# Kernel tuning notes

Hardware: AMD Instinct MI355X
Metric: run time of the kernel (lower is better)

Reference implementation:

```python
import jax, jax.numpy as jnp
import numpy as np

N = 8  # fixed node count per sample (hardcoded in the torch module)


def setup_inputs() -> dict:
    key = jax.random.key(0)
    ks = jax.random.split(key, 13)
    B = 131072

    def w(k, shape, fan_in):
        # torch nn.Linear default init: U(-1/sqrt(fan_in), 1/sqrt(fan_in))
        return jax.random.uniform(k, shape, jnp.float32, -1.0, 1.0) / np.sqrt(fan_in).astype(np.float32)

    return {
        "x": jax.random.normal(ks[0], (B, N), jnp.float32),
        "enc_w1": w(ks[1], (3, 64), 3),   "enc_b1": w(ks[2], (64,), 3),
        "enc_w2": w(ks[3], (64, 2), 64),  "enc_b2": w(ks[4], (2,), 64),
        "gcn1_w": w(ks[5], (2, 32), 2),   "gcn1_b": w(ks[6], (32,), 2),
        "gcn2_w": w(ks[7], (32, 32), 32), "gcn2_b": w(ks[8], (32,), 32),
        "dec_w1": w(ks[9], (32, 64), 32), "dec_b1": w(ks[10], (64,), 32),
        "dec_w2": w(ks[11], (64, 3), 64), "dec_b2": w(ks[12], (3,), 64),
    }


def _gabriel_norm_adj(p):
    """Batched Gabriel graph -> GCN-normalized (A + I) with unit edge weights.

    p: (B, N, 2) latent 2D points.
    Edge (i,j) exists iff no other point k lies strictly inside the circle
    with diameter (p_i, p_j)  (dist(p_k, mid)^2 < r^2, matching torch's '<').
    Gabriel graphs contain the nearest-neighbor graph, so for N>=2 edges always
    exist and the torch fallback branch is unreachable.
    Returns D^{-1/2} (A + I) D^{-1/2} of shape (B, N, N) (GCNConv default:
    add_self_loops=True with weight 1, symmetric normalization).
    """
    mid = (p[:, :, None, :] + p[:, None, :, :]) * 0.5                 # (B,N,N,2)
    r2 = jnp.sum((p[:, :, None, :] - mid) ** 2, axis=-1)              # (B,N,N)
    # d2[b,i,j,k] = ||p[b,k] - mid[b,i,j]||^2  -> (B,N,N,N), the big intermediate
    d2 = jnp.sum((p[:, None, None, :, :] - mid[:, :, :, None, :]) ** 2, axis=-1)
    a = jnp.arange(N)
    k_not_ij = (a[None, None, :] != a[:, None, None]) & (a[None, None, :] != a[None, :, None])  # (N,N,N) [i,j,k]
    blocked = jnp.any((d2 < r2[..., None]) & k_not_ij, axis=-1)       # (B,N,N)
    off_diag = a[:, None] != a[None, :]
    adj = ((~blocked) & off_diag).astype(p.dtype)                     # symmetric Gabriel adjacency
    a_hat = adj + jnp.eye(N, dtype=p.dtype)                           # self-loops, weight 1
    dinv = jax.lax.rsqrt(jnp.sum(a_hat, axis=-1))                     # (B,N)
    return dinv[:, :, None] * a_hat * dinv[:, None, :]


def reference(x, enc_w1, enc_b1, enc_w2, enc_b2,
              gcn1_w, gcn1_b, gcn2_w, gcn2_b,
              dec_w1, dec_b1, dec_w2, dec_b2):
    B = x.shape[0]
    idx = jnp.arange(N, dtype=x.dtype)
    # preprocess: (B, N, 3) rows [0, value, index]
    xp = jnp.stack([jnp.zeros_like(x), x, jnp.broadcast_to(idx, x.shape)], axis=-1)
    latent = jax.nn.relu(xp @ enc_w1 + enc_b1) @ enc_w2 + enc_b2      # (B,N,2)
    # torch builds the graph from detach().cpu().numpy() -> no grad through structure
    norm = jax.lax.stop_gradient(_gabriel_norm_adj(latent))           # (B,N,N)
    h1 = jax.nn.relu(jnp.einsum('bij,bjf->bif', norm, latent @ gcn1_w) + gcn1_b)  # (B,N,32)
    h2 = jnp.einsum('bij,bjf->bif', norm, h1 @ gcn2_w) + gcn2_b                    # (B,N,32)
    pooled = jnp.mean(h2, axis=1)                                     # (B,32)
    node = jnp.broadcast_to(pooled[:, None, :], (B, N, pooled.shape[-1]))
    dec = jax.nn.relu(node @ dec_w1 + dec_b1) @ dec_w2 + dec_b2       # (B,N,3)
    reconstructed = dec[:, :, 1]                                      # (B,N)
    return reconstructed, latent
```

## Files before the change

kernel.cpp:

```cpp
#include <hip/hip_runtime.h>


typedef float v2 __attribute__((ext_vector_type(2)));
static __device__ __forceinline__ v2 sp(float s) { return (v2){s, s}; }
static __device__ __forceinline__ v2 fma2(v2 a, v2 b, v2 c) {
    return __builtin_elementwise_fma(a, b, c);
}
static __device__ __forceinline__ v2 ldv2(const float* p) {
    return *reinterpret_cast<const v2*>(p);
}

__global__ __launch_bounds__(256) void gae_aux(
    const float* __restrict__ gcn2_w, const float* __restrict__ gcn2_b,
    const float* __restrict__ dec_w1, const float* __restrict__ dec_b1,
    const float* __restrict__ dec_w2, const float* __restrict__ enc_w1,
    const float* __restrict__ enc_b1, float* __restrict__ ws)
{
    const int tid = blockIdx.x * 256 + threadIdx.x;
    const int f = tid >> 6, h = tid & 63;
    float acc = 0.0f;
    #pragma unroll 8
    for (int g = 0; g < 32; ++g)
        acc = fmaf(gcn2_w[f * 32 + g], dec_w1[g * 64 + h], acc);
    ws[f * 64 + h] = acc;
    if (tid < 64) {
        float c = dec_b1[h];
        #pragma unroll 8
        for (int g = 0; g < 32; ++g)
            c = fmaf(gcn2_b[g], dec_w1[g * 64 + h], c);
        ws[2048 + h] = c;
        ws[2112 + h] = dec_w2[h * 3 + 1];
    }
    if (tid < 512) {
        const int hh = tid >> 3, ii = tid & 7;
        ws[2176 + tid] = fmaf((float)ii, enc_w1[128 + hh], enc_b1[hh]);
    }
}

template <int I, int J>
static __device__ __forceinline__ void gpair(const v2* __restrict__ p,
                                             unsigned& ml, unsigned& mh)
{
    #pragma clang fp contract(off)
    v2 mid = (p[I] + p[J]) * sp(0.5f);
    v2 di = p[I] - mid;  v2 si = di * di;  float r2i = si.x + si.y;
    v2 dj = p[J] - mid;  v2 sj = dj * dj;  float r2j = sj.x + sj.y;
    float dmin = 3.4e38f;
    #pragma unroll
    for (int k = 0; k < 8; ++k) {
        if (k == I || k == J) continue;
        v2 dk = p[k] - mid;
        v2 sk = dk * dk;
        dmin = fminf(dmin, sk.x + sk.y);
    }
    constexpr unsigned bi = 1u << (((I & 3) * 8) + J);
    constexpr unsigned bj = 1u << (((J & 3) * 8) + I);
    if (I < 4) ml |= (dmin < r2i) ? 0u : bi; else mh |= (dmin < r2i) ? 0u : bi;
    if (J < 4) ml |= (dmin < r2j) ? 0u : bj; else mh |= (dmin < r2j) ? 0u : bj;
}

__global__ __launch_bounds__(256, 8) void gae_main(
    const float* __restrict__ x,
    const float* __restrict__ enc_w1,
    const float* __restrict__ enc_w2,
    const float* __restrict__ enc_b2,
    const float* __restrict__ gcn1_w,
    const float* __restrict__ gcn1_b,
    const float* __restrict__ ws,
    const float* __restrict__ dec_b2,
    float* __restrict__ out_rec,
    float* __restrict__ out_lat,
    int B)
{
    __shared__ union { v2 p[8][64]; v2 t[16][64]; } ptb;
    __shared__ union { unsigned m[4][2][64]; float o[4][64]; } mob;
    __shared__ v2    nbuf[8][64];
    __shared__ float cjbuf[8][64];

    const int lane = threadIdx.x & 63;
    const int ru   = __builtin_amdgcn_readfirstlane(threadIdx.x >> 6);
    int g = blockIdx.x * 64 + lane;
    if (g >= B) g = B - 1;

    const float2 xr = *reinterpret_cast<const float2*>(x + (size_t)g * 8 + 2 * ru);
    const v2 xp2 = (v2){xr.x, xr.y};

    const float* ctab = ws + 2176;
    v2 pl0, pl1;
    { const v2 b2v = ldv2(enc_b2); pl0 = b2v; pl1 = b2v; }
    #pragma unroll 8
    for (int h = 0; h < 64; ++h) {
        const float wx = enc_w1[64 + h];
        const v2 uxy = ldv2(enc_w2 + 2 * h);
        const v2 cpr = ldv2(ctab + h * 8 + 2 * ru);
        v2 t = fma2(xp2, sp(wx), cpr);
        float t0 = fmaxf(t.x, 0.0f);
        float t1 = fmaxf(t.y, 0.0f);
        pl0 = fma2(sp(t0), uxy, pl0);
        pl1 = fma2(sp(t1), uxy, pl1);
    }

    *reinterpret_cast<float4*>(out_lat + (size_t)g * 16 + 4 * ru) =
        make_float4(pl0.x, pl0.y, pl1.x, pl1.y);

    ptb.p[2 * ru + 0][lane] = pl0;
    ptb.p[2 * ru + 1][lane] = pl1;
    __syncthreads();
    v2 p[8];
    #pragma unroll
    for (int j = 0; j < 8; ++j) p[j] = ptb.p[j][lane];

    unsigned ml = 0u, mh = 0u;
    if (ru == 0) {
        gpair<0,1>(p, ml, mh); gpair<0,2>(p, ml, mh); gpair<0,3>(p, ml, mh);
        gpair<0,4>(p, ml, mh); gpair<0,5>(p, ml, mh); gpair<0,6>(p, ml, mh);
        gpair<0,7>(p, ml, mh);
    } else if (ru == 1) {
        gpair<1,2>(p, ml, mh); gpair<1,3>(p, ml, mh); gpair<1,4>(p, ml, mh);
        gpair<1,5>(p, ml, mh); gpair<1,6>(p, ml, mh); gpair<1,7>(p, ml, mh);
        gpair<2,3>(p, ml, mh);
    } else if (ru == 2) {
        gpair<2,4>(p, ml, mh); gpair<2,5>(p, ml, mh); gpair<2,6>(p, ml, mh);
        gpair<2,7>(p, ml, mh); gpair<3,4>(p, ml, mh); gpair<3,5>(p, ml, mh);
        gpair<3,6>(p, ml, mh);
    } else {
        gpair<3,7>(p, ml, mh); gpair<4,5>(p, ml, mh); gpair<4,6>(p, ml, mh);
        gpair<4,7>(p, ml, mh); gpair<5,6>(p, ml, mh); gpair<5,7>(p, ml, mh);
        gpair<6,7>(p, ml, mh);
    }

    mob.m[ru][0][lane] = ml;
    mob.m[ru][1][lane] = mh;
    __syncthreads();
    ml = (mob.m[0][0][lane] | mob.m[1][0][lane]) |
         (mob.m[2][0][lane] | mob.m[3][0][lane]) | 0x08040201u;
    mh = (mob.m[0][1][lane] | mob.m[1][1][lane]) |
         (mob.m[2][1][lane] | mob.m[3][1][lane]) | 0x80402010u;

    float dinv[8];
    v2 q[8];
    #pragma unroll
    for (int i = 0; i < 8; ++i) {
        const unsigned rb = ((i < 4 ? ml : mh) >> ((i & 3) * 8)) & 0xffu;
        dinv[i] = __builtin_amdgcn_rsqf((float)__popc(rb));
        q[i] = sp(dinv[i]) * p[i];
    }

    {
        const unsigned w = (ru < 2) ? ml : mh;
        const int sh = ((2 * ru) & 3) * 8;
        const unsigned rb0 = (w >> sh) & 0xffu;
        const unsigned rb1 = (w >> (sh + 8)) & 0xffu;
        const float dv0 = __builtin_amdgcn_rsqf((float)__popc(rb0));
        const float dv1 = __builtin_amdgcn_rsqf((float)__popc(rb1));
        v2 a0 = sp(0.0f), a1 = sp(0.0f);
        #pragma unroll
        for (int j = 0; j < 8; ++j) {
            a0 = fma2(sp((float)((rb0 >> j) & 1u)), q[j], a0);
            a1 = fma2(sp((float)((rb1 >> j) & 1u)), q[j], a1);
        }
        nbuf[2 * ru + 0][lane] = sp(dv0) * a0;
        nbuf[2 * ru + 1][lane] = sp(dv1) * a1;

        const int j0 = 2 * ru, j1 = 2 * ru + 1;
        float s0 = 0.0f, s1 = 0.0f;
        #pragma unroll
        for (int i = 0; i < 8; ++i) {
            const unsigned rb = ((i < 4 ? ml : mh) >> ((i & 3) * 8)) & 0xffu;
            s0 = fmaf((float)((rb >> j0) & 1u), dinv[i], s0);
            s1 = fmaf((float)((rb >> j1) & 1u), dinv[i], s1);
        }
        cjbuf[j0][lane] = 0.125f * dv0 * s0;
        cjbuf[j1][lane] = 0.125f * dv1 * s1;
    }
    __syncthreads();

    const float* w0 = gcn1_w + 8 * ru;
    const float* w1 = gcn1_w + 32 + 8 * ru;
    const float* bl = gcn1_b + 8 * ru;
    v2 t2[4];
    #pragma unroll
    for (int fp = 0; fp < 4; ++fp) t2[fp] = sp(0.0f);
    #pragma unroll
    for (int i = 0; i < 8; ++i) {
        const v2 ni = nbuf[i][lane];
        const float ci = cjbuf[i][lane];
        const v2 nxi = sp(ni.x), nyi = sp(ni.y), civ = sp(ci);
        #pragma unroll
        for (int fp = 0; fp < 4; ++fp) {
            v2 h = fma2(nxi, ldv2(w0 + 2 * fp),
                   fma2(nyi, ldv2(w1 + 2 * fp), ldv2(bl + 2 * fp)));
            h = __builtin_elementwise_max(h, sp(0.0f));
            t2[fp] = fma2(civ, h, t2[fp]);
        }
    }

    #pragma unroll
    for (int fp = 0; fp < 4; ++fp) ptb.t[4 * ru + fp][lane] = t2[fp];
    __syncthreads();

    const float* Wd = ws + 16 * ru;
    const float* cd = ws + 2048 + 16 * ru;
    const float* w2 = ws + 2112 + 16 * ru;
    v2 a2[8];
    #pragma unroll
    for (int hp = 0; hp < 8; ++hp) a2[hp] = ldv2(cd + 2 * hp);
    #pragma unroll
    for (int fp = 0; fp < 16; ++fp) {
        const v2 tv = ptb.t[fp][lane];
        const float* wrA = Wd + (2 * fp) * 64;
        const float* wrB = Wd + (2 * fp + 1) * 64;
        const v2 tA = sp(tv.x), tB = sp(tv.y);
        #pragma unroll
        for (int hp = 0; hp < 8; ++hp) {
            a2[hp] = fma2(tA, ldv2(wrA + 2 * hp), a2[hp]);
            a2[hp] = fma2(tB, ldv2(wrB + 2 * hp), a2[hp]);
        }
    }
    v2 oacc = sp(0.0f);
    #pragma unroll
    for (int hp = 0; hp < 8; ++hp) {
        v2 rr = __builtin_elementwise_max(a2[hp], sp(0.0f));
        oacc = fma2(rr, ldv2(w2 + 2 * hp), oacc);
    }
    const float opart = oacc.x + oacc.y;

    mob.o[ru][lane] = opart;
    __syncthreads();
    const float outv = ((mob.o[0][lane] + mob.o[1][lane]) +
                        (mob.o[2][lane] + mob.o[3][lane])) + dec_b2[1];

    *reinterpret_cast<float2*>(out_rec + (size_t)g * 8 + 2 * ru) =
        make_float2(outv, outv);
}

extern "C" void kernel_launch(void* const* d_in, const int* in_sizes, int n_in,
                              void* d_out, int out_size, void* d_ws, size_t ws_size,
                              hipStream_t stream) {
    const float* x       = (const float*)d_in[0];
    const float* enc_w1  = (const float*)d_in[1];
    const float* enc_b1  = (const float*)d_in[2];
    const float* enc_w2  = (const float*)d_in[3];
    const float* enc_b2  = (const float*)d_in[4];
    const float* gcn1_w  = (const float*)d_in[5];
    const float* gcn1_b  = (const float*)d_in[6];
    const float* gcn2_w  = (const float*)d_in[7];
    const float* gcn2_b  = (const float*)d_in[8];
    const float* dec_w1  = (const float*)d_in[9];
    const float* dec_b1  = (const float*)d_in[10];
    const float* dec_w2  = (const float*)d_in[11];
    const float* dec_b2  = (const float*)d_in[12];

    const int B = in_sizes[0] / 8;
    float* out_rec = (float*)d_out;
    float* out_lat = out_rec + (size_t)B * 8;
    float* ws      = (float*)d_ws;

    gae_aux<<<8, 256, 0, stream>>>(gcn2_w, gcn2_b, dec_w1, dec_b1, dec_w2,
                                   enc_w1, enc_b1, ws);

    const int blocks = (B + 63) / 64;
    gae_main<<<blocks, 256, 0, stream>>>(
        x, enc_w1, enc_w2, enc_b2,
        gcn1_w, gcn1_b, ws, dec_b2,
        out_rec, out_lat, B);
}
```

Baseline: 107.0 us.

## Split encoder into separate kernel and reload latents from global in GCN kernel

Moves the encoder MLP out of the fused main kernel into its own kernel that writes latents to global memory, and the GCN/decoder kernel then reads all eight points per sample directly from global instead of exchanging them through shared memory with a barrier. It also computes the index-dependent encoder bias inline rather than from a precomputed workspace table, and raises wave priority during the decoder FMA loop. This adds a kernel launch and a global round trip of the latent tensor, in exchange for simpler kernels with fewer barriers and possibly better occupancy.

```diff
diff --git a/kernel.cpp b/kernel.cpp
--- a/kernel.cpp
+++ b/kernel.cpp
@@ -13,8 +13,7 @@
 __global__ __launch_bounds__(256) void gae_aux(
     const float* __restrict__ gcn2_w, const float* __restrict__ gcn2_b,
     const float* __restrict__ dec_w1, const float* __restrict__ dec_b1,
-    const float* __restrict__ dec_w2, const float* __restrict__ enc_w1,
-    const float* __restrict__ enc_b1, float* __restrict__ ws)
+    const float* __restrict__ dec_w2, float* __restrict__ ws)
 {
     const int tid = blockIdx.x * 256 + threadIdx.x;
     const int f = tid >> 6, h = tid & 63;
@@ -31,10 +30,43 @@
         ws[2048 + h] = c;
         ws[2112 + h] = dec_w2[h * 3 + 1];
     }
-    if (tid < 512) {
-        const int hh = tid >> 3, ii = tid & 7;
-        ws[2176 + tid] = fmaf((float)ii, enc_w1[128 + hh], enc_b1[hh]);
-    }
+}
+
+__global__ __launch_bounds__(256, 8) void gae_enc(
+    const float* __restrict__ x,
+    const float* __restrict__ enc_w1,
+    const float* __restrict__ enc_b1,
+    const float* __restrict__ enc_w2,
+    const float* __restrict__ enc_b2,
+    float* __restrict__ out_lat,
+    int nthreads)
+{
+    const int t = blockIdx.x * 256 + threadIdx.x;
+    if (t >= nthreads) return;
+
+    const float2 xr = *reinterpret_cast<const float2*>(x + (size_t)t * 2);
+    const v2 xp2 = (v2){xr.x, xr.y};
+    const float i0 = (float)(2 * (t & 3));
+    const float i1 = i0 + 1.0f;
+
+    v2 pl0, pl1;
+    { const v2 b2v = ldv2(enc_b2); pl0 = b2v; pl1 = b2v; }
+    #pragma unroll 8
+    for (int h = 0; h < 64; ++h) {
+        const float wx = enc_w1[64 + h];
+        const float wi = enc_w1[128 + h];
+        const float bb = enc_b1[h];
+        const v2 uxy = ldv2(enc_w2 + 2 * h);
+        const float c0 = fmaf(i0, wi, bb);
+        const float c1 = fmaf(i1, wi, bb);
+        v2 tt = fma2(xp2, sp(wx), (v2){c0, c1});
+        float t0 = fmaxf(tt.x, 0.0f);
+        float t1 = fmaxf(tt.y, 0.0f);
+        pl0 = fma2(sp(t0), uxy, pl0);
+        pl1 = fma2(sp(t1), uxy, pl1);
+    }
+    *reinterpret_cast<float4*>(out_lat + (size_t)t * 4) =
+        make_float4(pl0.x, pl0.y, pl1.x, pl1.y);
 }
 
 template <int I, int J>
@@ -59,56 +91,34 @@
     if (J < 4) ml |= (dmin < r2j) ? 0u : bj; else mh |= (dmin < r2j) ? 0u : bj;
 }
 
-__global__ __launch_bounds__(256, 8) void gae_main(
-    const float* __restrict__ x,
-    const float* __restrict__ enc_w1,
-    const float* __restrict__ enc_w2,
-    const float* __restrict__ enc_b2,
+__global__ __launch_bounds__(256, 8) void gae_gcn(
+    const float* __restrict__ lat,
     const float* __restrict__ gcn1_w,
     const float* __restrict__ gcn1_b,
     const float* __restrict__ ws,
     const float* __restrict__ dec_b2,
     float* __restrict__ out_rec,
-    float* __restrict__ out_lat,
     int B)
 {
-    __shared__ union { v2 p[8][64]; v2 t[16][64]; } ptb;
-    __shared__ union { unsigned m[4][2][64]; float o[4][64]; } mob;
-    __shared__ v2    nbuf[8][64];
-    __shared__ float cjbuf[8][64];
+    __shared__ v2 tbuf[16][64];
+    __shared__ unsigned mbuf[4][2][64];
+    __shared__ union { struct { v2 n[8][64]; float cj[8][64]; } nc;
+                       float o[4][64]; } u;
 
     const int lane = threadIdx.x & 63;
     const int ru   = __builtin_amdgcn_readfirstlane(threadIdx.x >> 6);
     int g = blockIdx.x * 64 + lane;
     if (g >= B) g = B - 1;
 
-    const float2 xr = *reinterpret_cast<const float2*>(x + (size_t)g * 8 + 2 * ru);
-    const v2 xp2 = (v2){xr.x, xr.y};
-
-    const float* ctab = ws + 2176;
-    v2 pl0, pl1;
-    { const v2 b2v = ldv2(enc_b2); pl0 = b2v; pl1 = b2v; }
-    #pragma unroll 8
-    for (int h = 0; h < 64; ++h) {
-        const float wx = enc_w1[64 + h];
-        const v2 uxy = ldv2(enc_w2 + 2 * h);
-        const v2 cpr = ldv2(ctab + h * 8 + 2 * ru);
-        v2 t = fma2(xp2, sp(wx), cpr);
-        float t0 = fmaxf(t.x, 0.0f);
-        float t1 = fmaxf(t.y, 0.0f);
-        pl0 = fma2(sp(t0), uxy, pl0);
-        pl1 = fma2(sp(t1), uxy, pl1);
-    }
-
-    *reinterpret_cast<float4*>(out_lat + (size_t)g * 16 + 4 * ru) =
-        make_float4(pl0.x, pl0.y, pl1.x, pl1.y);
-
-    ptb.p[2 * ru + 0][lane] = pl0;
-    ptb.p[2 * ru + 1][lane] = pl1;
-    __syncthreads();
     v2 p[8];
-    #pragma unroll
-    for (int j = 0; j < 8; ++j) p[j] = ptb.p[j][lane];
+    {
+        const float4* lp = reinterpret_cast<const float4*>(lat + (size_t)g * 16);
+        float4 a = lp[0], b = lp[1], c = lp[2], d = lp[3];
+        p[0] = (v2){a.x, a.y}; p[1] = (v2){a.z, a.w};
+        p[2] = (v2){b.x, b.y}; p[3] = (v2){b.z, b.w};
+        p[4] = (v2){c.x, c.y}; p[5] = (v2){c.z, c.w};
+        p[6] = (v2){d.x, d.y}; p[7] = (v2){d.z, d.w};
+    }
 
     unsigned ml = 0u, mh = 0u;
     if (ru == 0) {
@@ -129,13 +139,13 @@
         gpair<6,7>(p, ml, mh);
     }
 
-    mob.m[ru][0][lane] = ml;
-    mob.m[ru][1][lane] = mh;
-    __syncthreads();
-    ml = (mob.m[0][0][lane] | mob.m[1][0][lane]) |
-         (mob.m[2][0][lane] | mob.m[3][0][lane]) | 0x08040201u;
-    mh = (mob.m[0][1][lane] | mob.m[1][1][lane]) |
-         (mob.m[2][1][lane] | mob.m[3][1][lane]) | 0x80402010u;
+    mbuf[ru][0][lane] = ml;
+    mbuf[ru][1][lane] = mh;
+    __syncthreads();
+    ml = (mbuf[0][0][lane] | mbuf[1][0][lane]) |
+         (mbuf[2][0][lane] | mbuf[3][0][lane]) | 0x08040201u;
+    mh = (mbuf[0][1][lane] | mbuf[1][1][lane]) |
+         (mbuf[2][1][lane] | mbuf[3][1][lane]) | 0x80402010u;
 
     float dinv[8];
     v2 q[8];
@@ -159,8 +169,8 @@
             a0 = fma2(sp((float)((rb0 >> j) & 1u)), q[j], a0);
             a1 = fma2(sp((float)((rb1 >> j) & 1u)), q[j], a1);
         }
-        nbuf[2 * ru + 0][lane] = sp(dv0) * a0;
-        nbuf[2 * ru + 1][lane] = sp(dv1) * a1;
+        u.nc.n[2 * ru + 0][lane] = sp(dv0) * a0;
+        u.nc.n[2 * ru + 1][lane] = sp(dv1) * a1;
 
         const int j0 = 2 * ru, j1 = 2 * ru + 1;
         float s0 = 0.0f, s1 = 0.0f;
@@ -170,8 +180,8 @@
             s0 = fmaf((float)((rb >> j0) & 1u), dinv[i], s0);
             s1 = fmaf((float)((rb >> j1) & 1u), dinv[i], s1);
         }
-        cjbuf[j0][lane] = 0.125f * dv0 * s0;
-        cjbuf[j1][lane] = 0.125f * dv1 * s1;
+        u.nc.cj[j0][lane] = 0.125f * dv0 * s0;
+        u.nc.cj[j1][lane] = 0.125f * dv1 * s1;
     }
     __syncthreads();
 
@@ -183,8 +193,8 @@
     for (int fp = 0; fp < 4; ++fp) t2[fp] = sp(0.0f);
     #pragma unroll
     for (int i = 0; i < 8; ++i) {
-        const v2 ni = nbuf[i][lane];
-        const float ci = cjbuf[i][lane];
+        const v2 ni = u.nc.n[i][lane];
+        const float ci = u.nc.cj[i][lane];
         const v2 nxi = sp(ni.x), nyi = sp(ni.y), civ = sp(ci);
         #pragma unroll
         for (int fp = 0; fp < 4; ++fp) {
@@ -196,7 +206,7 @@
     }
 
     #pragma unroll
-    for (int fp = 0; fp < 4; ++fp) ptb.t[4 * ru + fp][lane] = t2[fp];
+    for (int fp = 0; fp < 4; ++fp) tbuf[4 * ru + fp][lane] = t2[fp];
     __syncthreads();
 
     const float* Wd = ws + 16 * ru;
@@ -205,9 +215,10 @@
     v2 a2[8];
     #pragma unroll
     for (int hp = 0; hp < 8; ++hp) a2[hp] = ldv2(cd + 2 * hp);
+    __builtin_amdgcn_s_setprio(1);
     #pragma unroll
     for (int fp = 0; fp < 16; ++fp) {
-        const v2 tv = ptb.t[fp][lane];
+        const v2 tv = tbuf[fp][lane];
         const float* wrA = Wd + (2 * fp) * 64;
         const float* wrB = Wd + (2 * fp + 1) * 64;
         const v2 tA = sp(tv.x), tB = sp(tv.y);
@@ -217,6 +228,7 @@
             a2[hp] = fma2(tB, ldv2(wrB + 2 * hp), a2[hp]);
         }
     }
+    __builtin_amdgcn_s_setprio(0);
     v2 oacc = sp(0.0f);
     #pragma unroll
     for (int hp = 0; hp < 8; ++hp) {
@@ -225,10 +237,10 @@
     }
     const float opart = oacc.x + oacc.y;
 
-    mob.o[ru][lane] = opart;
-    __syncthreads();
-    const float outv = ((mob.o[0][lane] + mob.o[1][lane]) +
-                        (mob.o[2][lane] + mob.o[3][lane])) + dec_b2[1];
+    u.o[ru][lane] = opart;
+    __syncthreads();
+    const float outv = ((u.o[0][lane] + u.o[1][lane]) +
+                        (u.o[2][lane] + u.o[3][lane])) + dec_b2[1];
 
     *reinterpret_cast<float2*>(out_rec + (size_t)g * 8 + 2 * ru) =
         make_float2(outv, outv);
@@ -256,12 +268,13 @@
     float* out_lat = out_rec + (size_t)B * 8;
     float* ws      = (float*)d_ws;
 
-    gae_aux<<<8, 256, 0, stream>>>(gcn2_w, gcn2_b, dec_w1, dec_b1, dec_w2,
-                                   enc_w1, enc_b1, ws);
+    gae_aux<<<8, 256, 0, stream>>>(gcn2_w, gcn2_b, dec_w1, dec_b1, dec_w2, ws);
+
+    const int nthreads = 4 * B;
+    gae_enc<<<(nthreads + 255) / 256, 256, 0, stream>>>(
+        x, enc_w1, enc_b1, enc_w2, enc_b2, out_lat, nthreads);
 
     const int blocks = (B + 63) / 64;
-    gae_main<<<blocks, 256, 0, stream>>>(
-        x, enc_w1, enc_w2, enc_b2,
-        gcn1_w, gcn1_b, ws, dec_b2,
-        out_rec, out_lat, B);
-}
+    gae_gcn<<<blocks, 256, 0, stream>>>(
+        out_lat, gcn1_w, gcn1_b, ws, dec_b2, out_rec, B);
+}
```

Result: slower. 109.5 us (+2.3%).
